# Kernel optimization log

Measured on AMD Instinct MI355X. Metric: run time of the kernel, lower is better.

The kernel has to match this reference:

```python
import jax, jax.numpy as jnp
import numpy as np

N_NODES = 50000
N_EDGES = 800000
N_FEAT = 128
N_CLASSES = 64
K_HOPS = 2


def setup_inputs() -> dict:
    key = jax.random.key(0)
    k1, k2, k3, k4 = jax.random.split(key, 4)
    x = jax.random.normal(k1, (N_NODES, N_FEAT), dtype=jnp.float32)
    edge_index = jax.random.randint(k2, (2, N_EDGES), 0, N_NODES, dtype=jnp.int64)
    # Linear(num_features -> num_classes) params (PyG SGConv lin layer)
    lim = 1.0 / np.sqrt(N_FEAT)
    W = jax.random.uniform(k3, (N_CLASSES, N_FEAT), minval=-lim, maxval=lim, dtype=jnp.float32)
    b = jax.random.uniform(k4, (N_CLASSES,), minval=-lim, maxval=lim, dtype=jnp.float32)
    return {"x": x, "edge_index": edge_index, "W": W, "b": b}


def reference(x, edge_index, W, b):
    N = x.shape[0]
    # gcn_norm: add self-loops, symmetric normalization deg^-1/2 A_hat deg^-1/2
    loop = jnp.arange(N, dtype=edge_index.dtype)
    src = jnp.concatenate([edge_index[0], loop])  # message sources j
    dst = jnp.concatenate([edge_index[1], loop])  # message targets i
    deg = jax.ops.segment_sum(jnp.ones_like(src, dtype=x.dtype), dst, num_segments=N)
    dinv = jnp.where(deg > 0, jax.lax.rsqrt(deg), 0.0)
    norm = dinv[src] * dinv[dst]  # [E+N]
    # K=2 hops of SpMM: out[i] = sum_{j->i} norm * x[j]
    for _ in range(K_HOPS):
        x = jax.ops.segment_sum(norm[:, None] * x[src], dst, num_segments=N)
    logits = x @ W.T + b  # [N, num_classes]
    return jax.nn.log_softmax(logits, axis=1)
```

## Files before the change

kernel.cpp:

```cpp
#include <hip/hip_runtime.h>
#include <hip/hip_fp16.h>
#include <math.h>

#define NFEAT 128
#define NCLS  64
#define RQ8   8
#define WSTR  132
#define NBLK  256


typedef _Float16 h2v __attribute__((ext_vector_type(2)));

__device__ __forceinline__ float dot2acc(unsigned int hv, unsigned int wv, float c) {
#if __has_builtin(__builtin_amdgcn_fdot2)
    union { unsigned int u; h2v v; } a, bq; a.u = hv; bq.u = wv;
    return __builtin_amdgcn_fdot2(a.v, bq.v, c, false);
#else
    union { unsigned int u; __half2 h; } a, bq; a.u = hv; bq.u = wv;
    float2 fa = __half22float2(a.h), fb = __half22float2(bq.h);
    return fmaf(fa.x, fb.x, fmaf(fa.y, fb.y, c));
#endif
}

__device__ __forceinline__ void acc4(__half2 a[4], uint4 v) {
    union { uint4 u; __half2 h[4]; } c; c.u = v;
    a[0] = __hadd2(a[0], c.h[0]); a[1] = __hadd2(a[1], c.h[1]);
    a[2] = __hadd2(a[2], c.h[2]); a[3] = __hadd2(a[3], c.h[3]);
}

__device__ __forceinline__ __half2 red8(__half2 a) {
    union { __half2 h; int i; } u, v;
    u.h = a; v.i = __shfl_xor(u.i, 8);  a = __hadd2(a, v.h);
    u.h = a; v.i = __shfl_xor(u.i, 16); a = __hadd2(a, v.h);
    u.h = a; v.i = __shfl_xor(u.i, 32); a = __hadd2(a, v.h);
    return a;
}

__global__ __launch_bounds__(256) void hist_kernel(const int* __restrict__ dst,
                                                   int* __restrict__ h,
                                                   int E4, int E, int nb) {
    __shared__ int lh[256];
    const int tid = threadIdx.x;
    lh[tid] = 0;
    __syncthreads();
    for (int idx = blockIdx.x * 256 + tid; idx < E4; idx += NBLK * 256) {
        int base = idx * 4;
        if (base + 3 < E) {
            int4 d = ((const int4*)dst)[idx];
            atomicAdd(&lh[d.x >> 8], 1); atomicAdd(&lh[d.y >> 8], 1);
            atomicAdd(&lh[d.z >> 8], 1); atomicAdd(&lh[d.w >> 8], 1);
        } else {
            for (int e = base; e < E; ++e) atomicAdd(&lh[dst[e] >> 8], 1);
        }
    }
    __syncthreads();
    if (tid < nb) h[blockIdx.x * nb + tid] = lh[tid];
}

__global__ __launch_bounds__(256) void colscan_kernel(int* __restrict__ h,
                                                      int* __restrict__ btot, int nb) {
    __shared__ int lds[256];
    const int tid = threadIdx.x;
    const int B = blockIdx.x;
    int v = h[tid * nb + B];
    lds[tid] = v;
    __syncthreads();
    for (int off = 1; off < 256; off <<= 1) {
        int t = (tid >= off) ? lds[tid - off] : 0;
        __syncthreads();
        lds[tid] += t;
        __syncthreads();
    }
    h[tid * nb + B] = lds[tid] - v;
    if (tid == 255) btot[B] = lds[255];
}

__global__ __launch_bounds__(256) void bucket_scan_kernel(const int* __restrict__ btot,
                                                          int* __restrict__ bbase, int nb) {
    __shared__ int lds[256];
    const int tid = threadIdx.x;
    int v = (tid < nb) ? btot[tid] : 0;
    lds[tid] = v;
    __syncthreads();
    for (int off = 1; off < 256; off <<= 1) {
        int t = (tid >= off) ? lds[tid - off] : 0;
        __syncthreads();
        lds[tid] += t;
        __syncthreads();
    }
    if (tid < nb) bbase[tid + 1] = lds[tid];
    if (tid == 0) bbase[0] = 0;
}

__global__ __launch_bounds__(256) void bucket_scatter_kernel(const int* __restrict__ src,
                                                             const int* __restrict__ dst,
                                                             const int* __restrict__ h,
                                                             const int* __restrict__ bbase,
                                                             int2* __restrict__ bedg,
                                                             int E4, int E, int nb) {
    __shared__ int cur[256];
    const int tid = threadIdx.x;
    if (tid < nb) cur[tid] = bbase[tid] + h[blockIdx.x * nb + tid];
    __syncthreads();
    for (int idx = blockIdx.x * 256 + tid; idx < E4; idx += NBLK * 256) {
        int base = idx * 4;
        if (base + 3 < E) {
            int4 s = ((const int4*)src)[idx];
            int4 d = ((const int4*)dst)[idx];
            int p;
            p = atomicAdd(&cur[d.x >> 8], 1); bedg[p] = make_int2(s.x, d.x);
            p = atomicAdd(&cur[d.y >> 8], 1); bedg[p] = make_int2(s.y, d.y);
            p = atomicAdd(&cur[d.z >> 8], 1); bedg[p] = make_int2(s.z, d.z);
            p = atomicAdd(&cur[d.w >> 8], 1); bedg[p] = make_int2(s.w, d.w);
        } else {
            for (int e = base; e < E; ++e) {
                int p = atomicAdd(&cur[dst[e] >> 8], 1);
                bedg[p] = make_int2(src[e], dst[e]);
            }
        }
    }
}

__global__ __launch_bounds__(256) void drain_kernel(const int2* __restrict__ bedg,
                                                    const int* __restrict__ bbase,
                                                    int* __restrict__ csr,
                                                    int* __restrict__ rbeg,
                                                    int* __restrict__ rend,
                                                    float* __restrict__ dinv, int N) {
    __shared__ int lcnt[256];
    __shared__ int lds[256];
    __shared__ int loc[256];
    const int B = blockIdx.x;
    const int tid = threadIdx.x;
    const int s0 = bbase[B], s1 = bbase[B + 1];

    lcnt[tid] = 0;
    __syncthreads();
    for (int e = s0 + tid; e < s1; e += 256)
        atomicAdd(&lcnt[bedg[e].y & 255], 1);
    __syncthreads();

    const int c = lcnt[tid];
    const int cp = (c + 7) & ~7;
    lds[tid] = cp;
    __syncthreads();
    for (int off = 1; off < 256; off <<= 1) {
        int t = (tid >= off) ? lds[tid - off] : 0;
        __syncthreads();
        lds[tid] += t;
        __syncthreads();
    }
    const int base = bbase[B] + 1792 * B;
    loc[tid] = base + lds[tid] - cp;
    __syncthreads();
    lcnt[tid] = loc[tid];
    __syncthreads();

    for (int e = s0 + tid; e < s1; e += 256) {
        int2 Ev = bedg[e];
        int p = atomicAdd(&lcnt[Ev.y & 255], 1);
        csr[p] = Ev.x;
    }
    __syncthreads();

    int i = B * 256 + tid;
    if (i < N) {
        int start = loc[tid], end = start + cp;
        for (int p = lcnt[tid]; p < end; ++p) csr[p] = N;
        rbeg[i] = start; rend[i] = end;
        dinv[i] = rsqrtf((float)c + 1.0f);
    }
}

__global__ __launch_bounds__(512) void gemm_kernel(const float* __restrict__ x,
                                                   const float* __restrict__ W,
                                                   const float* __restrict__ dinv,
                                                   __half* __restrict__ zh,
                                                   __half* __restrict__ y1h, int N) {
    __shared__ __half Wl[NCLS * WSTR];
    __shared__ __align__(16) __half HT[64][NFEAT];

    const int tid = threadIdx.x;
    const int w = tid >> 6, lane = tid & 63;

    if (blockIdx.x == 0 && tid < 32) {
        if (tid < 16) ((uint2*)zh)[(size_t)N * 16 + tid] = uint2{0u, 0u};
        else          ((uint2*)y1h)[(size_t)N * 16 + (tid - 16)] = uint2{0u, 0u};
    }

    for (int e = tid; e < NCLS * NFEAT; e += 512) {
        int r = e >> 7, c = e & 127;
        Wl[r * WSTR + c] = __float2half(W[e]);
    }
    {
        const float4* srcf = (const float4*)(x + (size_t)blockIdx.x * 64 * NFEAT);
        uint2* dh = (uint2*)&HT[0][0];
        const int row0 = blockIdx.x * 64;
        #pragma unroll
        for (int t = 0; t < 4; ++t) {
            int e = tid + 512 * t;
            float4 f = (row0 + (e >> 5) < N) ? srcf[e] : float4{0.f, 0.f, 0.f, 0.f};
            union { uint2 u; __half2 h[2]; } r;
            r.h[0] = __floats2half2_rn(f.x, f.y);
            r.h[1] = __floats2half2_rn(f.z, f.w);
            dh[e] = r.u;
        }
    }
    __syncthreads();

    unsigned int wreg[64];
    {
        const uint2* wr = (const uint2*)&Wl[lane * WSTR];
        #pragma unroll
        for (int t = 0; t < 32; ++t) {
            uint2 v = wr[t];
            wreg[2 * t] = v.x; wreg[2 * t + 1] = v.y;
        }
    }

    #pragma unroll 1
    for (int r = 0; r < 8; ++r) {
        int node = blockIdx.x * 64 + w * 8 + r;
        if (node >= N) break;
        const unsigned int* hrow = (const unsigned int*)&HT[w * 8 + r][0];
        float dot = 0.f;
        #pragma unroll
        for (int t = 0; t < 64; ++t)
            dot = dot2acc(hrow[t], wreg[t], dot);
        zh[(size_t)node * NCLS + lane] = __float2half(dinv[node] * dot);
    }
}

__device__ __forceinline__ void gather_row64(__half2 a[4], const uint4* __restrict__ X,
                                             const int* __restrict__ csr,
                                             int ks, int ke, int sub, int q, int Nd) {
    int k = ks;
    int j0, j1, j2, j3;
    bool have = (k + 32 <= ke);
    if (have) {
        j0 = csr[k + sub];      j1 = csr[k + 8 + sub];
        j2 = csr[k + 16 + sub]; j3 = csr[k + 24 + sub];
    }
    while (have) {
        uint4 v0 = X[(size_t)j0 * RQ8 + q];
        uint4 v1 = X[(size_t)j1 * RQ8 + q];
        uint4 v2 = X[(size_t)j2 * RQ8 + q];
        uint4 v3 = X[(size_t)j3 * RQ8 + q];
        k += 32;
        have = (k + 32 <= ke);
        if (have) {
            j0 = csr[k + sub];      j1 = csr[k + 8 + sub];
            j2 = csr[k + 16 + sub]; j3 = csr[k + 24 + sub];
        }
        acc4(a, v0); acc4(a, v1); acc4(a, v2); acc4(a, v3);
    }
    int rem = (ke - k) >> 3;
    if (rem) {
        int t0 = csr[k + sub];
        int t1 = csr[k + 8 + sub];
        int t2 = csr[k + 16 + sub];
        if (rem < 2) t1 = Nd;
        if (rem < 3) t2 = Nd;
        uint4 v0 = X[(size_t)t0 * RQ8 + q];
        uint4 v1 = X[(size_t)t1 * RQ8 + q];
        uint4 v2 = X[(size_t)t2 * RQ8 + q];
        acc4(a, v0); acc4(a, v1); acc4(a, v2);
    }
}

template <int SQUARE>
__global__ __launch_bounds__(256) void hop64_kernel(const __half* __restrict__ in_h,
                                                    const float* __restrict__ dinv,
                                                    const int* __restrict__ rbeg,
                                                    const int* __restrict__ rend,
                                                    const int* __restrict__ csr,
                                                    __half* __restrict__ out_h, int N) {
    const int tid = threadIdx.x;
    const int w = tid >> 6, lane = tid & 63;
    const int i = blockIdx.x * 4 + w;
    if (i >= N) return;
    const int sub = lane >> 3;
    const int q = lane & 7;
    const uint4* X = (const uint4*)in_h;

    __half2 a[4];
    a[0] = __float2half2_rn(0.f); a[1] = a[0]; a[2] = a[0]; a[3] = a[0];

    int ks = rbeg[i], ke = rend[i];
    gather_row64(a, X, csr, ks, ke, sub, q, N);
    if (sub == 0) acc4(a, X[(size_t)i * RQ8 + q]);

    a[0] = red8(a[0]); a[1] = red8(a[1]); a[2] = red8(a[2]); a[3] = red8(a[3]);

    if (sub == 0) {
        float di = dinv[i];
        float s = SQUARE ? di * di : di;
        union { uint4 u; __half2 h[4]; } r;
        #pragma unroll
        for (int t = 0; t < 4; ++t) {
            float2 f = __half22float2(a[t]);
            r.h[t] = __floats2half2_rn(s * f.x, s * f.y);
        }
        ((uint4*)out_h)[(size_t)i * RQ8 + q] = r.u;
    }
}

__global__ __launch_bounds__(256) void hop2cls_kernel(const __half* __restrict__ in_h,
                                                      const float* __restrict__ dinv,
                                                      const int* __restrict__ rbeg,
                                                      const int* __restrict__ rend,
                                                      const int* __restrict__ csr,
                                                      const float* __restrict__ b,
                                                      float* __restrict__ out, int N) {
    const int tid = threadIdx.x;
    const int w = tid >> 6, lane = tid & 63;
    const int i = blockIdx.x * 4 + w;
    if (i >= N) return;
    const int sub = lane >> 3;
    const int q = lane & 7;
    const uint4* X = (const uint4*)in_h;

    float4 b0 = ((const float4*)b)[q * 2];
    float4 b1 = ((const float4*)b)[q * 2 + 1];

    __half2 a[4];
    a[0] = __float2half2_rn(0.f); a[1] = a[0]; a[2] = a[0]; a[3] = a[0];

    int ks = rbeg[i], ke = rend[i];
    gather_row64(a, X, csr, ks, ke, sub, q, N);
    if (sub == 0) acc4(a, X[(size_t)i * RQ8 + q]);

    a[0] = red8(a[0]); a[1] = red8(a[1]); a[2] = red8(a[2]); a[3] = red8(a[3]);

    if (sub == 0) {
        float di = dinv[i];
        float f[8];
        float2 p;
        p = __half22float2(a[0]); f[0] = fmaf(di, p.x, b0.x); f[1] = fmaf(di, p.y, b0.y);
        p = __half22float2(a[1]); f[2] = fmaf(di, p.x, b0.z); f[3] = fmaf(di, p.y, b0.w);
        p = __half22float2(a[2]); f[4] = fmaf(di, p.x, b1.x); f[5] = fmaf(di, p.y, b1.y);
        p = __half22float2(a[3]); f[6] = fmaf(di, p.x, b1.z); f[7] = fmaf(di, p.y, b1.w);
        float m = f[0];
        #pragma unroll
        for (int t = 1; t < 8; ++t) m = fmaxf(m, f[t]);
        m = fmaxf(m, __shfl_xor(m, 1));
        m = fmaxf(m, __shfl_xor(m, 2));
        m = fmaxf(m, __shfl_xor(m, 4));
        float se = 0.f;
        #pragma unroll
        for (int t = 0; t < 8; ++t) se += __expf(f[t] - m);
        se += __shfl_xor(se, 1);
        se += __shfl_xor(se, 2);
        se += __shfl_xor(se, 4);
        float ls = m + logf(se);
        float4 o0 = {f[0] - ls, f[1] - ls, f[2] - ls, f[3] - ls};
        float4 o1 = {f[4] - ls, f[5] - ls, f[6] - ls, f[7] - ls};
        float4* op = (float4*)(out + (size_t)i * NCLS);
        op[q * 2] = o0; op[q * 2 + 1] = o1;
    }
}


static inline size_t align256(size_t v) { return (v + 255) & ~(size_t)255; }

extern "C" void kernel_launch(void* const* d_in, const int* in_sizes, int n_in,
                              void* d_out, int out_size, void* d_ws, size_t ws_size,
                              hipStream_t stream) {
    const float* x  = (const float*)d_in[0];
    const int*   ei = (const int*)d_in[1];
    const float* W  = (const float*)d_in[2];
    const float* b  = (const float*)d_in[3];
    float* out = (float*)d_out;

    const int N = in_sizes[0] / NFEAT;
    const int E = in_sizes[1] / 2;
    const int* src = ei;
    const int* dst = ei + E;
    const int NBUCK = (N + 255) >> 8;

    const int CSR_CAP = E + 1792 * NBUCK + 64;

    char* ws = (char*)d_ws;
    size_t o = 0;
    int*    h     = (int*)(ws + o);    o += align256((size_t)NBLK * NBUCK * 4);
    int*    btot  = (int*)(ws + o);    o += align256(256 * 4);
    int*    bbase = (int*)(ws + o);    o += align256(257 * 4);
    int2*   bedg  = (int2*)(ws + o);   o += align256((size_t)E * 8);
    int*    csr   = (int*)(ws + o);    o += align256((size_t)CSR_CAP * 4);
    int*    rbeg  = (int*)(ws + o);    o += align256((size_t)N * 4);
    int*    rend  = (int*)(ws + o);    o += align256((size_t)N * 4);
    float*  dinv  = (float*)(ws + o);  o += align256((size_t)N * 4);
    __half* zh    = (__half*)(ws + o); o += align256((size_t)(N + 1) * NCLS * 2);
    __half* y1h   = (__half*)(ws + o); o += align256((size_t)(N + 1) * NCLS * 2);

    const int E4 = (E + 3) / 4;

    hist_kernel<<<NBLK, 256, 0, stream>>>(dst, h, E4, E, NBUCK);
    colscan_kernel<<<NBUCK, 256, 0, stream>>>(h, btot, NBUCK);
    bucket_scan_kernel<<<1, 256, 0, stream>>>(btot, bbase, NBUCK);
    bucket_scatter_kernel<<<NBLK, 256, 0, stream>>>(src, dst, h, bbase, bedg, E4, E, NBUCK);
    drain_kernel<<<NBUCK, 256, 0, stream>>>(bedg, bbase, csr, rbeg, rend, dinv, N);
    gemm_kernel<<<(N + 63) / 64, 512, 0, stream>>>(x, W, dinv, zh, y1h, N);
    hop64_kernel<1><<<(N + 3) / 4, 256, 0, stream>>>(zh, dinv, rbeg, rend, csr, y1h, N);
    hop2cls_kernel<<<(N + 3) / 4, 256, 0, stream>>>(y1h, dinv, rbeg, rend, csr, b, out, N);
}
```

Before: 161.4 us.

## Build CSR via global per-node atomics and fold self-loop into row

```diff
diff --git a/kernel.cpp b/kernel.cpp
--- a/kernel.cpp
+++ b/kernel.cpp
@@ -36,34 +36,67 @@
     return a;
 }
 
-__global__ __launch_bounds__(256) void hist_kernel(const int* __restrict__ dst,
-                                                   int* __restrict__ h,
-                                                   int E4, int E, int nb) {
-    __shared__ int lh[256];
-    const int tid = threadIdx.x;
-    lh[tid] = 0;
-    __syncthreads();
-    for (int idx = blockIdx.x * 256 + tid; idx < E4; idx += NBLK * 256) {
+__global__ __launch_bounds__(256) void zero_kernel(int4* __restrict__ p, int n4) {
+    int i = blockIdx.x * 256 + threadIdx.x;
+    if (i < n4) p[i] = int4{0, 0, 0, 0};
+}
+
+__global__ __launch_bounds__(256) void deg_kernel(const int* __restrict__ dst,
+                                                  int* __restrict__ deg,
+                                                  int E4, int E) {
+    for (int idx = blockIdx.x * 256 + threadIdx.x; idx < E4; idx += NBLK * 256) {
         int base = idx * 4;
         if (base + 3 < E) {
             int4 d = ((const int4*)dst)[idx];
-            atomicAdd(&lh[d.x >> 8], 1); atomicAdd(&lh[d.y >> 8], 1);
-            atomicAdd(&lh[d.z >> 8], 1); atomicAdd(&lh[d.w >> 8], 1);
+            atomicAdd(&deg[d.x], 1); atomicAdd(&deg[d.y], 1);
+            atomicAdd(&deg[d.z], 1); atomicAdd(&deg[d.w], 1);
         } else {
-            for (int e = base; e < E; ++e) atomicAdd(&lh[dst[e] >> 8], 1);
-        }
-    }
-    __syncthreads();
-    if (tid < nb) h[blockIdx.x * nb + tid] = lh[tid];
-}
-
-__global__ __launch_bounds__(256) void colscan_kernel(int* __restrict__ h,
-                                                      int* __restrict__ btot, int nb) {
+            for (int e = base; e < E; ++e) atomicAdd(&deg[dst[e]], 1);
+        }
+    }
+}
+
+__global__ __launch_bounds__(256) void rowsum_kernel(const int* __restrict__ deg,
+                                                     int* __restrict__ btot, int N) {
     __shared__ int lds[256];
     const int tid = threadIdx.x;
+    int i = blockIdx.x * 256 + tid;
+    int cp = (i < N) ? ((deg[i] + 8) & ~7) : 0;
+    lds[tid] = cp;
+    __syncthreads();
+    for (int off = 128; off > 0; off >>= 1) {
+        if (tid < off) lds[tid] += lds[tid + off];
+        __syncthreads();
+    }
+    if (tid == 0) btot[blockIdx.x] = lds[0];
+}
+
+__global__ __launch_bounds__(256) void rowscan_kernel(const int* __restrict__ deg,
+                                                      const int* __restrict__ btot,
+                                                      int* __restrict__ rbeg,
+                                                      int* __restrict__ rend,
+                                                      int* __restrict__ cur,
+                                                      float* __restrict__ dinv,
+                                                      int* __restrict__ csr, int N) {
+    __shared__ int lds[256];
+    __shared__ int base_s;
+    const int tid = threadIdx.x;
     const int B = blockIdx.x;
-    int v = h[tid * nb + B];
-    lds[tid] = v;
+
+    lds[tid] = (tid < B) ? btot[tid] : 0;
+    __syncthreads();
+    for (int off = 128; off > 0; off >>= 1) {
+        if (tid < off) lds[tid] += lds[tid + off];
+        __syncthreads();
+    }
+    if (tid == 0) base_s = lds[0];
+    __syncthreads();
+    const int base = base_s;
+
+    int i = B * 256 + tid;
+    int d  = (i < N) ? deg[i] : 0;
+    int cp = (i < N) ? ((d + 8) & ~7) : 0;
+    lds[tid] = cp;
     __syncthreads();
     for (int off = 1; off < 256; off <<= 1) {
         int t = (tid >= off) ? lds[tid - off] : 0;
@@ -71,104 +104,38 @@
         lds[tid] += t;
         __syncthreads();
     }
-    h[tid * nb + B] = lds[tid] - v;
-    if (tid == 255) btot[B] = lds[255];
-}
-
-__global__ __launch_bounds__(256) void bucket_scan_kernel(const int* __restrict__ btot,
-                                                          int* __restrict__ bbase, int nb) {
-    __shared__ int lds[256];
-    const int tid = threadIdx.x;
-    int v = (tid < nb) ? btot[tid] : 0;
-    lds[tid] = v;
-    __syncthreads();
-    for (int off = 1; off < 256; off <<= 1) {
-        int t = (tid >= off) ? lds[tid - off] : 0;
-        __syncthreads();
-        lds[tid] += t;
-        __syncthreads();
-    }
-    if (tid < nb) bbase[tid + 1] = lds[tid];
-    if (tid == 0) bbase[0] = 0;
-}
-
-__global__ __launch_bounds__(256) void bucket_scatter_kernel(const int* __restrict__ src,
-                                                             const int* __restrict__ dst,
-                                                             const int* __restrict__ h,
-                                                             const int* __restrict__ bbase,
-                                                             int2* __restrict__ bedg,
-                                                             int E4, int E, int nb) {
-    __shared__ int cur[256];
-    const int tid = threadIdx.x;
-    if (tid < nb) cur[tid] = bbase[tid] + h[blockIdx.x * nb + tid];
-    __syncthreads();
-    for (int idx = blockIdx.x * 256 + tid; idx < E4; idx += NBLK * 256) {
+    if (i < N) {
+        int start = base + lds[tid] - cp;
+        rbeg[i] = start;
+        rend[i] = start + cp;
+        cur[i]  = start;
+        dinv[i] = rsqrtf((float)d + 1.0f);
+        csr[start + d] = i;
+        for (int p = start + d + 1; p < start + cp; ++p) csr[p] = N;
+    }
+}
+
+__global__ __launch_bounds__(256) void scatter_csr_kernel(const int* __restrict__ src,
+                                                          const int* __restrict__ dst,
+                                                          int* __restrict__ cur,
+                                                          int* __restrict__ csr,
+                                                          int E4, int E) {
+    for (int idx = blockIdx.x * 256 + threadIdx.x; idx < E4; idx += NBLK * 256) {
         int base = idx * 4;
         if (base + 3 < E) {
             int4 s = ((const int4*)src)[idx];
             int4 d = ((const int4*)dst)[idx];
             int p;
-            p = atomicAdd(&cur[d.x >> 8], 1); bedg[p] = make_int2(s.x, d.x);
-            p = atomicAdd(&cur[d.y >> 8], 1); bedg[p] = make_int2(s.y, d.y);
-            p = atomicAdd(&cur[d.z >> 8], 1); bedg[p] = make_int2(s.z, d.z);
-            p = atomicAdd(&cur[d.w >> 8], 1); bedg[p] = make_int2(s.w, d.w);
+            p = atomicAdd(&cur[d.x], 1); csr[p] = s.x;
+            p = atomicAdd(&cur[d.y], 1); csr[p] = s.y;
+            p = atomicAdd(&cur[d.z], 1); csr[p] = s.z;
+            p = atomicAdd(&cur[d.w], 1); csr[p] = s.w;
         } else {
             for (int e = base; e < E; ++e) {
-                int p = atomicAdd(&cur[dst[e] >> 8], 1);
-                bedg[p] = make_int2(src[e], dst[e]);
+                int p = atomicAdd(&cur[dst[e]], 1);
+                csr[p] = src[e];
             }
         }
-    }
-}
-
-__global__ __launch_bounds__(256) void drain_kernel(const int2* __restrict__ bedg,
-                                                    const int* __restrict__ bbase,
-                                                    int* __restrict__ csr,
-                                                    int* __restrict__ rbeg,
-                                                    int* __restrict__ rend,
-                                                    float* __restrict__ dinv, int N) {
-    __shared__ int lcnt[256];
-    __shared__ int lds[256];
-    __shared__ int loc[256];
-    const int B = blockIdx.x;
-    const int tid = threadIdx.x;
-    const int s0 = bbase[B], s1 = bbase[B + 1];
-
-    lcnt[tid] = 0;
-    __syncthreads();
-    for (int e = s0 + tid; e < s1; e += 256)
-        atomicAdd(&lcnt[bedg[e].y & 255], 1);
-    __syncthreads();
-
-    const int c = lcnt[tid];
-    const int cp = (c + 7) & ~7;
-    lds[tid] = cp;
-    __syncthreads();
-    for (int off = 1; off < 256; off <<= 1) {
-        int t = (tid >= off) ? lds[tid - off] : 0;
-        __syncthreads();
-        lds[tid] += t;
-        __syncthreads();
-    }
-    const int base = bbase[B] + 1792 * B;
-    loc[tid] = base + lds[tid] - cp;
-    __syncthreads();
-    lcnt[tid] = loc[tid];
-    __syncthreads();
-
-    for (int e = s0 + tid; e < s1; e += 256) {
-        int2 Ev = bedg[e];
-        int p = atomicAdd(&lcnt[Ev.y & 255], 1);
-        csr[p] = Ev.x;
-    }
-    __syncthreads();
-
-    int i = B * 256 + tid;
-    if (i < N) {
-        int start = loc[tid], end = start + cp;
-        for (int p = lcnt[tid]; p < end; ++p) csr[p] = N;
-        rbeg[i] = start; rend[i] = end;
-        dinv[i] = rsqrtf((float)c + 1.0f);
     }
 }
 
@@ -288,7 +255,6 @@
 
     int ks = rbeg[i], ke = rend[i];
     gather_row64(a, X, csr, ks, ke, sub, q, N);
-    if (sub == 0) acc4(a, X[(size_t)i * RQ8 + q]);
 
     a[0] = red8(a[0]); a[1] = red8(a[1]); a[2] = red8(a[2]); a[3] = red8(a[3]);
 
@@ -328,7 +294,6 @@
 
     int ks = rbeg[i], ke = rend[i];
     gather_row64(a, X, csr, ks, ke, sub, q, N);
-    if (sub == 0) acc4(a, X[(size_t)i * RQ8 + q]);
 
     a[0] = red8(a[0]); a[1] = red8(a[1]); a[2] = red8(a[2]); a[3] = red8(a[3]);
 
@@ -376,30 +341,30 @@
     const int E = in_sizes[1] / 2;
     const int* src = ei;
     const int* dst = ei + E;
-    const int NBUCK = (N + 255) >> 8;
-
-    const int CSR_CAP = E + 1792 * NBUCK + 64;
+    const int NB = (N + 255) >> 8;
+
+    const int CSR_CAP = E + 8 * N + 64;
 
     char* ws = (char*)d_ws;
     size_t o = 0;
-    int*    h     = (int*)(ws + o);    o += align256((size_t)NBLK * NBUCK * 4);
+    int*    deg   = (int*)(ws + o);    o += align256((size_t)((N + 3) & ~3) * 4);
     int*    btot  = (int*)(ws + o);    o += align256(256 * 4);
-    int*    bbase = (int*)(ws + o);    o += align256(257 * 4);
-    int2*   bedg  = (int2*)(ws + o);   o += align256((size_t)E * 8);
-    int*    csr   = (int*)(ws + o);    o += align256((size_t)CSR_CAP * 4);
     int*    rbeg  = (int*)(ws + o);    o += align256((size_t)N * 4);
     int*    rend  = (int*)(ws + o);    o += align256((size_t)N * 4);
+    int*    cur   = (int*)(ws + o);    o += align256((size_t)N * 4);
     float*  dinv  = (float*)(ws + o);  o += align256((size_t)N * 4);
+    int*    csr   = (int*)(ws + o);    o += align256((size_t)CSR_CAP * 4);
     __half* zh    = (__half*)(ws + o); o += align256((size_t)(N + 1) * NCLS * 2);
     __half* y1h   = (__half*)(ws + o); o += align256((size_t)(N + 1) * NCLS * 2);
 
     const int E4 = (E + 3) / 4;
-
-    hist_kernel<<<NBLK, 256, 0, stream>>>(dst, h, E4, E, NBUCK);
-    colscan_kernel<<<NBUCK, 256, 0, stream>>>(h, btot, NBUCK);
-    bucket_scan_kernel<<<1, 256, 0, stream>>>(btot, bbase, NBUCK);
-    bucket_scatter_kernel<<<NBLK, 256, 0, stream>>>(src, dst, h, bbase, bedg, E4, E, NBUCK);
-    drain_kernel<<<NBUCK, 256, 0, stream>>>(bedg, bbase, csr, rbeg, rend, dinv, N);
+    const int n4 = (N + 3) / 4;
+
+    zero_kernel<<<(n4 + 255) / 256, 256, 0, stream>>>((int4*)deg, n4);
+    deg_kernel<<<NBLK, 256, 0, stream>>>(dst, deg, E4, E);
+    rowsum_kernel<<<NB, 256, 0, stream>>>(deg, btot, N);
+    rowscan_kernel<<<NB, 256, 0, stream>>>(deg, btot, rbeg, rend, cur, dinv, csr, N);
+    scatter_csr_kernel<<<NBLK, 256, 0, stream>>>(src, dst, cur, csr, E4, E);
     gemm_kernel<<<(N + 63) / 64, 512, 0, stream>>>(x, W, dinv, zh, y1h, N);
     hop64_kernel<1><<<(N + 3) / 4, 256, 0, stream>>>(zh, dinv, rbeg, rend, csr, y1h, N);
     hop2cls_kernel<<<(N + 3) / 4, 256, 0, stream>>>(y1h, dinv, rbeg, rend, csr, b, out, N);
```

After: 231.8 us. 43.6% more time.

## Pack bucketed edges into 32-bit words, fold self-loop into CSR, drop scan kernel

Applied to the files above, without the earlier changes.

```diff
diff --git a/kernel.cpp b/kernel.cpp
--- a/kernel.cpp
+++ b/kernel.cpp
@@ -7,6 +7,7 @@
 #define RQ8   8
 #define WSTR  132
 #define NBLK  256
+#define BSLACK 2048
 
 
 typedef _Float16 h2v __attribute__((ext_vector_type(2)));
@@ -36,6 +37,29 @@
     return a;
 }
 
+__device__ __forceinline__ int block_excl_scan_256(int v, int tid, int* scratch, int* total) {
+    const int lane = tid & 63, wv = tid >> 6;
+    __syncthreads();
+    int x = v;
+    #pragma unroll
+    for (int off = 1; off < 64; off <<= 1) {
+        int y = __shfl_up(x, off);
+        if (lane >= off) x += y;
+    }
+    if (lane == 63) scratch[wv] = x;
+    __syncthreads();
+    if (wv == 0 && lane < 4) {
+        int t = scratch[lane];
+        int y = __shfl_up(t, 1); if (lane >= 1) t += y;
+        y = __shfl_up(t, 2);     if (lane >= 2) t += y;
+        scratch[4 + lane] = t;
+    }
+    __syncthreads();
+    int wbase = (wv == 0) ? 0 : scratch[4 + wv - 1];
+    if (total) *total = scratch[7];
+    return wbase + x - v;
+}
+
 __global__ __launch_bounds__(256) void hist_kernel(const int* __restrict__ dst,
                                                    int* __restrict__ h,
                                                    int E4, int E, int nb) {
@@ -59,48 +83,28 @@
 
 __global__ __launch_bounds__(256) void colscan_kernel(int* __restrict__ h,
                                                       int* __restrict__ btot, int nb) {
-    __shared__ int lds[256];
+    __shared__ int scratch[8];
     const int tid = threadIdx.x;
     const int B = blockIdx.x;
     int v = h[tid * nb + B];
-    lds[tid] = v;
-    __syncthreads();
-    for (int off = 1; off < 256; off <<= 1) {
-        int t = (tid >= off) ? lds[tid - off] : 0;
-        __syncthreads();
-        lds[tid] += t;
-        __syncthreads();
-    }
-    h[tid * nb + B] = lds[tid] - v;
-    if (tid == 255) btot[B] = lds[255];
-}
-
-__global__ __launch_bounds__(256) void bucket_scan_kernel(const int* __restrict__ btot,
-                                                          int* __restrict__ bbase, int nb) {
-    __shared__ int lds[256];
-    const int tid = threadIdx.x;
-    int v = (tid < nb) ? btot[tid] : 0;
-    lds[tid] = v;
-    __syncthreads();
-    for (int off = 1; off < 256; off <<= 1) {
-        int t = (tid >= off) ? lds[tid - off] : 0;
-        __syncthreads();
-        lds[tid] += t;
-        __syncthreads();
-    }
-    if (tid < nb) bbase[tid + 1] = lds[tid];
-    if (tid == 0) bbase[0] = 0;
+    int tot;
+    int pre = block_excl_scan_256(v, tid, scratch, &tot);
+    h[tid * nb + B] = pre;
+    if (tid == 0) btot[B] = tot;
 }
 
 __global__ __launch_bounds__(256) void bucket_scatter_kernel(const int* __restrict__ src,
                                                              const int* __restrict__ dst,
                                                              const int* __restrict__ h,
-                                                             const int* __restrict__ bbase,
-                                                             int2* __restrict__ bedg,
+                                                             const int* __restrict__ btot,
+                                                             unsigned int* __restrict__ bedg,
                                                              int E4, int E, int nb) {
     __shared__ int cur[256];
-    const int tid = threadIdx.x;
-    if (tid < nb) cur[tid] = bbase[tid] + h[blockIdx.x * nb + tid];
+    __shared__ int scratch[8];
+    const int tid = threadIdx.x;
+    int bt = (tid < nb) ? btot[tid] : 0;
+    int pre = block_excl_scan_256(bt, tid, scratch, nullptr);
+    if (tid < nb) cur[tid] = pre + h[blockIdx.x * nb + tid];
     __syncthreads();
     for (int idx = blockIdx.x * 256 + tid; idx < E4; idx += NBLK * 256) {
         int base = idx * 4;
@@ -108,65 +112,66 @@
             int4 s = ((const int4*)src)[idx];
             int4 d = ((const int4*)dst)[idx];
             int p;
-            p = atomicAdd(&cur[d.x >> 8], 1); bedg[p] = make_int2(s.x, d.x);
-            p = atomicAdd(&cur[d.y >> 8], 1); bedg[p] = make_int2(s.y, d.y);
-            p = atomicAdd(&cur[d.z >> 8], 1); bedg[p] = make_int2(s.z, d.z);
-            p = atomicAdd(&cur[d.w >> 8], 1); bedg[p] = make_int2(s.w, d.w);
+            p = atomicAdd(&cur[d.x >> 8], 1); bedg[p] = ((unsigned)s.x << 8) | (d.x & 255);
+            p = atomicAdd(&cur[d.y >> 8], 1); bedg[p] = ((unsigned)s.y << 8) | (d.y & 255);
+            p = atomicAdd(&cur[d.z >> 8], 1); bedg[p] = ((unsigned)s.z << 8) | (d.z & 255);
+            p = atomicAdd(&cur[d.w >> 8], 1); bedg[p] = ((unsigned)s.w << 8) | (d.w & 255);
         } else {
             for (int e = base; e < E; ++e) {
                 int p = atomicAdd(&cur[dst[e] >> 8], 1);
-                bedg[p] = make_int2(src[e], dst[e]);
+                bedg[p] = ((unsigned)src[e] << 8) | (dst[e] & 255);
             }
         }
     }
 }
 
-__global__ __launch_bounds__(256) void drain_kernel(const int2* __restrict__ bedg,
-                                                    const int* __restrict__ bbase,
+__global__ __launch_bounds__(256) void drain_kernel(const unsigned int* __restrict__ bedg,
+                                                    const int* __restrict__ btot,
                                                     int* __restrict__ csr,
                                                     int* __restrict__ rbeg,
                                                     int* __restrict__ rend,
-                                                    float* __restrict__ dinv, int N) {
+                                                    float* __restrict__ dinv,
+                                                    int N, int nb) {
     __shared__ int lcnt[256];
-    __shared__ int lds[256];
     __shared__ int loc[256];
+    __shared__ int scratch[8];
+    __shared__ int s0_s, s1_s;
     const int B = blockIdx.x;
     const int tid = threadIdx.x;
-    const int s0 = bbase[B], s1 = bbase[B + 1];
-
+
+    int bt = (tid < nb) ? btot[tid] : 0;
+    int pre = block_excl_scan_256(bt, tid, scratch, nullptr);
+    if (tid == B) { s0_s = pre; s1_s = pre + bt; }
     lcnt[tid] = 0;
     __syncthreads();
+    const int s0 = s0_s, s1 = s1_s;
+
     for (int e = s0 + tid; e < s1; e += 256)
-        atomicAdd(&lcnt[bedg[e].y & 255], 1);
+        atomicAdd(&lcnt[bedg[e] & 255u], 1);
     __syncthreads();
 
     const int c = lcnt[tid];
-    const int cp = (c + 7) & ~7;
-    lds[tid] = cp;
-    __syncthreads();
-    for (int off = 1; off < 256; off <<= 1) {
-        int t = (tid >= off) ? lds[tid - off] : 0;
-        __syncthreads();
-        lds[tid] += t;
-        __syncthreads();
-    }
-    const int base = bbase[B] + 1792 * B;
-    loc[tid] = base + lds[tid] - cp;
+    const int cp = (c + 8) & ~7;
+    int rpre = block_excl_scan_256(cp, tid, scratch, nullptr);
+    const int base = s0 + BSLACK * B;
+    loc[tid] = base + rpre;
     __syncthreads();
     lcnt[tid] = loc[tid];
     __syncthreads();
 
     for (int e = s0 + tid; e < s1; e += 256) {
-        int2 Ev = bedg[e];
-        int p = atomicAdd(&lcnt[Ev.y & 255], 1);
-        csr[p] = Ev.x;
+        unsigned int Ev = bedg[e];
+        int p = atomicAdd(&lcnt[Ev & 255u], 1);
+        csr[p] = (int)(Ev >> 8);
     }
     __syncthreads();
 
     int i = B * 256 + tid;
     if (i < N) {
         int start = loc[tid], end = start + cp;
-        for (int p = lcnt[tid]; p < end; ++p) csr[p] = N;
+        int q = lcnt[tid];
+        csr[q++] = i;
+        for (int p = q; p < end; ++p) csr[p] = N;
         rbeg[i] = start; rend[i] = end;
         dinv[i] = rsqrtf((float)c + 1.0f);
     }
@@ -288,7 +293,6 @@
 
     int ks = rbeg[i], ke = rend[i];
     gather_row64(a, X, csr, ks, ke, sub, q, N);
-    if (sub == 0) acc4(a, X[(size_t)i * RQ8 + q]);
 
     a[0] = red8(a[0]); a[1] = red8(a[1]); a[2] = red8(a[2]); a[3] = red8(a[3]);
 
@@ -328,7 +332,6 @@
 
     int ks = rbeg[i], ke = rend[i];
     gather_row64(a, X, csr, ks, ke, sub, q, N);
-    if (sub == 0) acc4(a, X[(size_t)i * RQ8 + q]);
 
     a[0] = red8(a[0]); a[1] = red8(a[1]); a[2] = red8(a[2]); a[3] = red8(a[3]);
 
@@ -378,28 +381,26 @@
     const int* dst = ei + E;
     const int NBUCK = (N + 255) >> 8;
 
-    const int CSR_CAP = E + 1792 * NBUCK + 64;
+    const int CSR_CAP = E + BSLACK * NBUCK + 64;
 
     char* ws = (char*)d_ws;
     size_t o = 0;
-    int*    h     = (int*)(ws + o);    o += align256((size_t)NBLK * NBUCK * 4);
-    int*    btot  = (int*)(ws + o);    o += align256(256 * 4);
-    int*    bbase = (int*)(ws + o);    o += align256(257 * 4);
-    int2*   bedg  = (int2*)(ws + o);   o += align256((size_t)E * 8);
-    int*    csr   = (int*)(ws + o);    o += align256((size_t)CSR_CAP * 4);
-    int*    rbeg  = (int*)(ws + o);    o += align256((size_t)N * 4);
-    int*    rend  = (int*)(ws + o);    o += align256((size_t)N * 4);
-    float*  dinv  = (float*)(ws + o);  o += align256((size_t)N * 4);
-    __half* zh    = (__half*)(ws + o); o += align256((size_t)(N + 1) * NCLS * 2);
-    __half* y1h   = (__half*)(ws + o); o += align256((size_t)(N + 1) * NCLS * 2);
+    int*          h     = (int*)(ws + o);          o += align256((size_t)NBLK * NBUCK * 4);
+    int*          btot  = (int*)(ws + o);          o += align256(256 * 4);
+    unsigned int* bedg  = (unsigned int*)(ws + o); o += align256((size_t)E * 4);
+    int*          csr   = (int*)(ws + o);          o += align256((size_t)CSR_CAP * 4);
+    int*          rbeg  = (int*)(ws + o);          o += align256((size_t)N * 4);
+    int*          rend  = (int*)(ws + o);          o += align256((size_t)N * 4);
+    float*        dinv  = (float*)(ws + o);        o += align256((size_t)N * 4);
+    __half*       zh    = (__half*)(ws + o);       o += align256((size_t)(N + 1) * NCLS * 2);
+    __half*       y1h   = (__half*)(ws + o);       o += align256((size_t)(N + 1) * NCLS * 2);
 
     const int E4 = (E + 3) / 4;
 
     hist_kernel<<<NBLK, 256, 0, stream>>>(dst, h, E4, E, NBUCK);
     colscan_kernel<<<NBUCK, 256, 0, stream>>>(h, btot, NBUCK);
-    bucket_scan_kernel<<<1, 256, 0, stream>>>(btot, bbase, NBUCK);
-    bucket_scatter_kernel<<<NBLK, 256, 0, stream>>>(src, dst, h, bbase, bedg, E4, E, NBUCK);
-    drain_kernel<<<NBUCK, 256, 0, stream>>>(bedg, bbase, csr, rbeg, rend, dinv, N);
+    bucket_scatter_kernel<<<NBLK, 256, 0, stream>>>(src, dst, h, btot, bedg, E4, E, NBUCK);
+    drain_kernel<<<NBUCK, 256, 0, stream>>>(bedg, btot, csr, rbeg, rend, dinv, N, NBUCK);
     gemm_kernel<<<(N + 63) / 64, 512, 0, stream>>>(x, W, dinv, zh, y1h, N);
     hop64_kernel<1><<<(N + 3) / 4, 256, 0, stream>>>(zh, dinv, rbeg, rend, csr, y1h, N);
     hop2cls_kernel<<<(N + 3) / 4, 256, 0, stream>>>(y1h, dinv, rbeg, rend, csr, b, out, N);
```

Measured after the change: 155.8 us. 1.04x faster.
